# Kernel optimization log

Measured on AMD Instinct MI355X. Metric: run time of the kernel, lower is better.

## Reference

```python
import jax, jax.numpy as jnp
import numpy as np

N_NODES = 100000
N_EDGES = 1600000
F_IN = 128
N_HEADS = 4
F_OUT = 32
NEG_SLOPE = 0.2


def setup_inputs() -> dict:
    key = jax.random.key(0)
    k_feat, k_src, k_dst, k_w, k_as, k_ad, k_res = jax.random.split(key, 7)
    feat = jax.random.normal(k_feat, (N_NODES, F_IN), dtype=jnp.float32)
    src = jax.random.randint(k_src, (N_EDGES,), 0, N_NODES, dtype=jnp.int32)
    dst = jax.random.randint(k_dst, (N_EDGES,), 0, N_NODES, dtype=jnp.int32)
    s = 1.0 / np.sqrt(F_IN)
    W = jax.random.normal(k_w, (F_IN, N_HEADS * F_OUT), dtype=jnp.float32) * s
    att_src = jax.random.normal(k_as, (N_HEADS, F_OUT), dtype=jnp.float32) * 0.1
    att_dst = jax.random.normal(k_ad, (N_HEADS, F_OUT), dtype=jnp.float32) * 0.1
    W_res = jax.random.normal(k_res, (F_IN, N_HEADS * F_OUT), dtype=jnp.float32) * s
    return {"feat": feat, "W": W, "att_src": att_src, "att_dst": att_dst,
            "W_res": W_res, "src": src, "dst": dst}


def reference(feat, W, att_src, att_dst, W_res, src, dst):
    N = feat.shape[0]
    H, Fo = att_src.shape
    # shared linear projection (GATConv, bias=False): [N, H, Fo]
    x = (feat @ W).reshape(N, H, Fo)
    # per-node attention logits: [N, H]
    a_s = jnp.einsum('nhf,hf->nh', x, att_src)
    a_d = jnp.einsum('nhf,hf->nh', x, att_dst)
    # edge-wise scores + LeakyReLU: [E, H]
    e = jax.nn.leaky_relu(a_s[src] + a_d[dst], negative_slope=NEG_SLOPE)
    # segment softmax over incoming edges of each dst node
    e_max = jax.ops.segment_max(e, dst, num_segments=N)  # [N, H]
    e_exp = jnp.exp(e - e_max[dst])                       # [E, H]
    denom = jax.ops.segment_sum(e_exp, dst, num_segments=N)  # [N, H]
    alpha = e_exp / denom[dst]                            # [E, H]
    # weighted scatter-add aggregation: [N, H, Fo]
    msg = x[src] * alpha[:, :, None]
    out = jax.ops.segment_sum(msg, dst, num_segments=N)
    # residual projection
    res = (feat @ W_res).reshape(N, H, Fo)
    return out + res
```

## Files before the change

### kernel.cpp

```cpp
#include <hip/hip_runtime.h>
#include <math.h>

#define NN 100000
#define NE 1600000
#define F_IN 128
#define C 128
#define NEG_SLOPE 0.2f
#define SCAN_NB ((NN + 1023) / 1024)
#define PROJ_NB ((NN + 63) / 64)
#define HIST_NB ((NE + 255) / 256)

typedef __attribute__((ext_vector_type(8))) short short8;
typedef __attribute__((ext_vector_type(4))) float f32x4;
typedef __attribute__((ext_vector_type(4))) float floatx4;
typedef __attribute__((ext_vector_type(4))) unsigned short ushortx4;

static __device__ __forceinline__ unsigned short f2bf(float f) {
    unsigned int u = __float_as_uint(f);
    unsigned int r = (u + 0x7fff + ((u >> 16) & 1)) >> 16;
    return (unsigned short)r;
}
static __device__ __forceinline__ float bf2f(unsigned short h) {
    return __uint_as_float((unsigned int)h << 16);
}

__global__ __launch_bounds__(256)
void wconv_kernel(const float* __restrict__ W,
                  const float* __restrict__ Wr,
                  unsigned short* __restrict__ Btf)
{
    int g = blockIdx.x * 256 + threadIdx.x;
    int nt = g >> 8;
    int kc = (g >> 6) & 3;
    int l  = g & 63;
    int n  = nt * 16 + (l & 15);
    int kb = kc * 32 + (l >> 4) * 8;
    unsigned short v[8];
    #pragma unroll
    for (int j = 0; j < 8; ++j) {
        int k = kb + j;
        float f = (n < 128) ? W[(size_t)k * 128 + n] : Wr[(size_t)k * 128 + (n - 128)];
        v[j] = f2bf(f);
    }
    *(short8*)&Btf[(size_t)g * 8] = *(short8*)v;
}

__global__ __launch_bounds__(256)
void proj_hist_kernel(const float* __restrict__ feat,
                      const unsigned short* __restrict__ Btf,
                      const float* __restrict__ att_src,
                      const float* __restrict__ att_dst,
                      const int* __restrict__ dst,
                      unsigned short* __restrict__ xb,
                      unsigned short* __restrict__ resb,
                      float* __restrict__ a_s,
                      float* __restrict__ a_d,
                      int* __restrict__ deg,
                      int* __restrict__ rank)
{
    __shared__ __align__(16) char smem[17408];
    __shared__ __align__(16) unsigned short Bs[16384];
    __shared__ float s_as[64][4];
    __shared__ float s_ad[64][4];
    const int tid = threadIdx.x;

    if (blockIdx.x >= PROJ_NB) {
        int e = (blockIdx.x - PROJ_NB) * 256 + tid;
        if (e < NE) rank[e] = atomicAdd(&deg[dst[e]], 1);
        return;
    }

    unsigned short* As = (unsigned short*)smem;
    const int base = blockIdx.x * 64;

    #pragma unroll
    for (int it = 0; it < 8; ++it) {
        int idx = it * 256 + tid;
        int row = idx >> 5;
        int c4  = idx & 31;
        int n = base + row;
        if (n < NN) {
            floatx4 f = __builtin_nontemporal_load(
                (const floatx4*)&feat[(size_t)n * F_IN + c4 * 4]);
            ushortx4 h;
            h.x = f2bf(f.x); h.y = f2bf(f.y); h.z = f2bf(f.z); h.w = f2bf(f.w);
            *(ushortx4*)&As[row * 136 + c4 * 4] = h;
        }
    }
    #pragma unroll
    for (int it = 0; it < 8; ++it) {
        int idx = it * 256 + tid;
        *(short8*)&Bs[idx * 8] = *(const short8*)&Btf[idx * 8];
    }
    __syncthreads();

    const int l = tid & 63;
    const int w = tid >> 6;
    const int quad = l >> 4;
    const int lo16 = l & 15;

    short8 af[4];
    const int arow = w * 16 + lo16;
    #pragma unroll
    for (int kc = 0; kc < 4; ++kc)
        af[kc] = *(const short8*)&As[arow * 136 + kc * 32 + quad * 8];

    f32x4 acc[16];
    #pragma unroll
    for (int nt = 0; nt < 16; ++nt) acc[nt] = (f32x4){0.f, 0.f, 0.f, 0.f};

    #pragma unroll
    for (int nt = 0; nt < 8; ++nt) {
        const unsigned short* bp = &Bs[(nt * 4) * 512 + l * 8];
        short8 b0 = *(const short8*)&bp[0];
        short8 b1 = *(const short8*)&bp[512];
        short8 b2 = *(const short8*)&bp[1024];
        short8 b3 = *(const short8*)&bp[1536];
        acc[nt] = __builtin_amdgcn_mfma_f32_16x16x32_bf16(af[0], b0, acc[nt], 0, 0, 0);
        acc[nt] = __builtin_amdgcn_mfma_f32_16x16x32_bf16(af[1], b1, acc[nt], 0, 0, 0);
        acc[nt] = __builtin_amdgcn_mfma_f32_16x16x32_bf16(af[2], b2, acc[nt], 0, 0, 0);
        acc[nt] = __builtin_amdgcn_mfma_f32_16x16x32_bf16(af[3], b3, acc[nt], 0, 0, 0);
    }

    __syncthreads();
    #pragma unroll
    for (int it = 0; it < 8; ++it) {
        int idx = it * 256 + tid;
        *(short8*)&Bs[idx * 8] = *(const short8*)&Btf[16384 + idx * 8];
    }
    __syncthreads();

    #pragma unroll
    for (int nt = 8; nt < 16; ++nt) {
        const unsigned short* bp = &Bs[((nt - 8) * 4) * 512 + l * 8];
        short8 b0 = *(const short8*)&bp[0];
        short8 b1 = *(const short8*)&bp[512];
        short8 b2 = *(const short8*)&bp[1024];
        short8 b3 = *(const short8*)&bp[1536];
        acc[nt] = __builtin_amdgcn_mfma_f32_16x16x32_bf16(af[0], b0, acc[nt], 0, 0, 0);
        acc[nt] = __builtin_amdgcn_mfma_f32_16x16x32_bf16(af[1], b1, acc[nt], 0, 0, 0);
        acc[nt] = __builtin_amdgcn_mfma_f32_16x16x32_bf16(af[2], b2, acc[nt], 0, 0, 0);
        acc[nt] = __builtin_amdgcn_mfma_f32_16x16x32_bf16(af[3], b3, acc[nt], 0, 0, 0);
    }

    float* T2 = (float*)smem + w * (16 * 68);
    const int g  = l >> 4;
    const int cf = (l & 15) * 4;

    #pragma unroll
    for (int p = 0; p < 2; ++p) {
        #pragma unroll
        for (int ntl = 0; ntl < 4; ++ntl) {
            int nt = p * 4 + ntl;
            #pragma unroll
            for (int r = 0; r < 4; ++r)
                T2[(quad * 4 + r) * 68 + ntl * 16 + lo16] = acc[nt][r];
        }
        floatx4 ws4 = *(const floatx4*)&att_src[p * 64 + cf];
        floatx4 wd4 = *(const floatx4*)&att_dst[p * 64 + cf];
        float ps[4], pd[4];
        #pragma unroll
        for (int it = 0; it < 4; ++it) {
            int row = it * 4 + g;
            floatx4 v = *(floatx4*)&T2[row * 68 + cf];
            int node = base + w * 16 + row;
            ushortx4 hh;
            hh.x = f2bf(v.x); hh.y = f2bf(v.y); hh.z = f2bf(v.z); hh.w = f2bf(v.w);
            if (node < NN)
                __builtin_nontemporal_store(hh,
                    (ushortx4*)&xb[(size_t)node * C + p * 64 + cf]);
            ps[it] = v.x * ws4.x + v.y * ws4.y + v.z * ws4.z + v.w * ws4.w;
            pd[it] = v.x * wd4.x + v.y * wd4.y + v.z * wd4.z + v.w * wd4.w;
        }
        #pragma unroll
        for (int it = 0; it < 4; ++it) {
            #pragma unroll
            for (int d = 1; d < 8; d <<= 1) {
                ps[it] += __shfl_xor(ps[it], d, 64);
                pd[it] += __shfl_xor(pd[it], d, 64);
            }
        }
        if ((l & 7) == 0) {
            int hh = p * 2 + ((l & 15) >> 3);
            #pragma unroll
            for (int it = 0; it < 4; ++it) {
                int lr = w * 16 + it * 4 + g;
                s_as[lr][hh] = ps[it];
                s_ad[lr][hh] = pd[it];
            }
        }
    }

    #pragma unroll
    for (int p = 0; p < 2; ++p) {
        #pragma unroll
        for (int ntl = 0; ntl < 4; ++ntl) {
            int nt = 8 + p * 4 + ntl;
            #pragma unroll
            for (int r = 0; r < 4; ++r)
                T2[(quad * 4 + r) * 68 + ntl * 16 + lo16] = acc[nt][r];
        }
        #pragma unroll
        for (int it = 0; it < 4; ++it) {
            int row = it * 4 + g;
            floatx4 v = *(floatx4*)&T2[row * 68 + cf];
            int node = base + w * 16 + row;
            ushortx4 hh;
            hh.x = f2bf(v.x); hh.y = f2bf(v.y); hh.z = f2bf(v.z); hh.w = f2bf(v.w);
            if (node < NN)
                __builtin_nontemporal_store(hh,
                    (ushortx4*)&resb[(size_t)node * C + p * 64 + cf]);
        }
    }

    __syncthreads();
    int idx = blockIdx.x * 256 + tid;
    if (idx < NN * 4) {
        a_s[idx] = ((float*)s_as)[tid];
        a_d[idx] = ((float*)s_ad)[tid];
    }
}

__global__ __launch_bounds__(1024)
void scan1_kernel(const int* __restrict__ deg, int* __restrict__ row_ptr,
                  int* __restrict__ bsum)
{
    __shared__ int wsum[16];
    const int t = threadIdx.x, lane = t & 63, wid = t >> 6;
    const int i = blockIdx.x * 1024 + t;
    int v0 = (i < NN) ? deg[i] : 0;
    int v = v0;
    #pragma unroll
    for (int off = 1; off < 64; off <<= 1) {
        int u = __shfl_up(v, off, 64);
        if (lane >= off) v += u;
    }
    if (lane == 63) wsum[wid] = v;
    __syncthreads();
    if (t == 0) {
        int run = 0;
        #pragma unroll
        for (int s = 0; s < 16; ++s) { int tmp = wsum[s]; wsum[s] = run; run += tmp; }
        bsum[blockIdx.x] = run;
    }
    __syncthreads();
    if (i < NN) row_ptr[i] = wsum[wid] + (v - v0);
}

__global__ __launch_bounds__(128)
void scan2_kernel(int* __restrict__ bsum)
{
    __shared__ int w0;
    const int t = threadIdx.x, lane = t & 63;
    int v0 = (t < SCAN_NB) ? bsum[t] : 0;
    int v = v0;
    #pragma unroll
    for (int off = 1; off < 64; off <<= 1) {
        int u = __shfl_up(v, off, 64);
        if (lane >= off) v += u;
    }
    if (t == 63) w0 = v;
    __syncthreads();
    int excl = (v - v0) + ((t >= 64) ? w0 : 0);
    if (t < SCAN_NB) bsum[t] = excl;
}

__global__ __launch_bounds__(1024)
void scan3_kernel(int* __restrict__ row_ptr, const int* __restrict__ bsum)
{
    const int i = blockIdx.x * 1024 + threadIdx.x;
    if (i < NN) row_ptr[i] = row_ptr[i] + bsum[i >> 10];
    if (i == 0) row_ptr[NN] = NE;
}

__global__ void scatter_kernel(const int* __restrict__ src,
                               const int* __restrict__ dst,
                               const int* __restrict__ rank,
                               const int* __restrict__ row_ptr,
                               int* __restrict__ csr_src)
{
    int e = blockIdx.x * blockDim.x + threadIdx.x;
    if (e < NE)
        csr_src[row_ptr[dst[e]] + rank[e]] = src[e];
}

__global__ __launch_bounds__(256)
void agg_kernel(const unsigned short* __restrict__ xb,
                const unsigned short* __restrict__ resb,
                const float* __restrict__ a_s,
                const float* __restrict__ a_d,
                const int* __restrict__ row_ptr,
                const int* __restrict__ csr_src,
                float* __restrict__ out)
{
    __shared__ float s_alpha[4][64 * 4];
    __shared__ int   s_srcs[4][64];
    const int tid = threadIdx.x;
    const int w = tid >> 6;
    const int l = tid & 63;
    const int n = blockIdx.x * 4 + w;
    if (n >= NN) return;
    const int r0  = row_ptr[n];
    const int deg = row_ptr[n + 1] - r0;

    const int half = l >> 5;
    const int hl   = l & 31;
    const int h    = hl >> 3;

    if (deg == 0) {
        if (half == 0) {
            ushort4 rv = *(const ushort4*)&resb[(size_t)n * C + hl * 4];
            floatx4 o;
            o.x = bf2f(rv.x); o.y = bf2f(rv.y);
            o.z = bf2f(rv.z); o.w = bf2f(rv.w);
            __builtin_nontemporal_store(o, (floatx4*)&out[(size_t)n * C + hl * 4]);
        }
        return;
    }

    const float4 ad4 = *(const float4*)&a_d[n * 4];

    float ax = 0.f, ay = 0.f, az = 0.f, aw = 0.f;
    float dx = 0.f, dy = 0.f, dz = 0.f, dw = 0.f;

    for (int c0 = 0; c0 < deg; c0 += 64) {
        int e = c0 + l;
        int s = 0;
        float4 ex = {0.f, 0.f, 0.f, 0.f};
        if (e < deg) {
            s = csr_src[r0 + e];
            float4 as4 = *(const float4*)&a_s[s * 4];
            float e0 = as4.x + ad4.x, e1 = as4.y + ad4.y;
            float e2 = as4.z + ad4.z, e3 = as4.w + ad4.w;
            e0 = (e0 > 0.f) ? e0 : NEG_SLOPE * e0;
            e1 = (e1 > 0.f) ? e1 : NEG_SLOPE * e1;
            e2 = (e2 > 0.f) ? e2 : NEG_SLOPE * e2;
            e3 = (e3 > 0.f) ? e3 : NEG_SLOPE * e3;
            ex.x = __expf(e0); ex.y = __expf(e1);
            ex.z = __expf(e2); ex.w = __expf(e3);
            dx += ex.x; dy += ex.y; dz += ex.z; dw += ex.w;
        }
        s_srcs[w][l] = s;
        *(float4*)&s_alpha[w][l * 4] = ex;

        int cn = min(64, deg - c0);
        int iters = (cn + 1) >> 1;
        #pragma unroll 2
        for (int i = 0; i < iters; ++i) {
            int ii = i * 2 + half;
            int   si = s_srcs[w][ii];
            float al = s_alpha[w][ii * 4 + h];
            ushort4 uv = *(const ushort4*)&xb[(size_t)si * C + hl * 4];
            ax = fmaf(al, bf2f(uv.x), ax);
            ay = fmaf(al, bf2f(uv.y), ay);
            az = fmaf(al, bf2f(uv.z), az);
            aw = fmaf(al, bf2f(uv.w), aw);
        }
    }

    #pragma unroll
    for (int d = 32; d > 0; d >>= 1) {
        dx += __shfl_xor(dx, d, 64);
        dy += __shfl_xor(dy, d, 64);
        dz += __shfl_xor(dz, d, 64);
        dw += __shfl_xor(dw, d, 64);
    }
    float den = (h == 0) ? dx : (h == 1) ? dy : (h == 2) ? dz : dw;
    float inv = 1.f / den;

    ax += __shfl_xor(ax, 32, 64);
    ay += __shfl_xor(ay, 32, 64);
    az += __shfl_xor(az, 32, 64);
    aw += __shfl_xor(aw, 32, 64);

    if (half == 0) {
        ushort4 rv = *(const ushort4*)&resb[(size_t)n * C + hl * 4];
        floatx4 o;
        o.x = bf2f(rv.x) + ax * inv;
        o.y = bf2f(rv.y) + ay * inv;
        o.z = bf2f(rv.z) + az * inv;
        o.w = bf2f(rv.w) + aw * inv;
        __builtin_nontemporal_store(o, (floatx4*)&out[(size_t)n * C + hl * 4]);
    }
}

extern "C" void kernel_launch(void* const* d_in, const int* in_sizes, int n_in,
                              void* d_out, int out_size, void* d_ws, size_t ws_size,
                              hipStream_t stream)
{
    const float* feat    = (const float*)d_in[0];
    const float* W       = (const float*)d_in[1];
    const float* att_src = (const float*)d_in[2];
    const float* att_dst = (const float*)d_in[3];
    const float* W_res   = (const float*)d_in[4];
    const int*   src     = (const int*)d_in[5];
    const int*   dst     = (const int*)d_in[6];
    float* out = (float*)d_out;

    char* p = (char*)d_ws;
    unsigned short* xb   = (unsigned short*)p; p += (size_t)NN * C * sizeof(unsigned short);
    unsigned short* resb = (unsigned short*)p; p += (size_t)NN * C * sizeof(unsigned short);
    unsigned short* Btf  = (unsigned short*)p; p += (size_t)256 * 128 * sizeof(unsigned short);
    float* a_s = (float*)p;            p += (size_t)NN * 4 * sizeof(float);
    float* a_d = (float*)p;            p += (size_t)NN * 4 * sizeof(float);
    int* deg     = (int*)p;            p += (size_t)NN * sizeof(int);
    int* row_ptr = (int*)p;            p += (size_t)(NN + 1) * sizeof(int);
    int* bsum    = (int*)p;            p += (size_t)256 * sizeof(int);
    int* rank    = (int*)p;            p += (size_t)NE * sizeof(int);
    int* csr_src = (int*)p;            p += (size_t)NE * sizeof(int);

    hipMemsetAsync(deg, 0, (size_t)NN * sizeof(int), stream);

    wconv_kernel<<<16, 256, 0, stream>>>(W, W_res, Btf);
    proj_hist_kernel<<<PROJ_NB + HIST_NB, 256, 0, stream>>>(
        feat, Btf, att_src, att_dst, dst, xb, resb, a_s, a_d, deg, rank);
    scan1_kernel<<<SCAN_NB, 1024, 0, stream>>>(deg, row_ptr, bsum);
    scan2_kernel<<<1, 128, 0, stream>>>(bsum);
    scan3_kernel<<<SCAN_NB, 1024, 0, stream>>>(row_ptr, bsum);
    scatter_kernel<<<(NE + 255) / 256, 256, 0, stream>>>(src, dst, rank, row_ptr, csr_src);
    agg_kernel<<<(NN + 3) / 4, 256, 0, stream>>>(xb, resb, a_s, a_d, row_ptr, csr_src, out);
}
```

Measured before the change: 313.0 us.

## Load projection operands directly from global and widen aggregation gathers to 16 bytes

The projection kernel no longer stages feat and weight tiles in LDS. Each lane loads its bf16 A fragment straight from global memory and reads B fragments from the pre-swizzled weight buffer, which removes several syncthreads and shrinks LDS so more blocks can be resident (launch bounds request 4). The aggregation kernel now has each lane gather 8 bf16 features (16-byte loads) while four edges are processed in parallel per wavefront, reduced afterwards with two cross-lane shuffles. The trade-off is redundant global or L2 reads of the weights by every wave, and more registers in the aggregation loop.

Result: slower. 324.8 us (+3.8%).

```diff
diff --git a/kernel.cpp b/kernel.cpp
--- a/kernel.cpp
+++ b/kernel.cpp
@@ -45,7 +45,7 @@
     *(short8*)&Btf[(size_t)g * 8] = *(short8*)v;
 }
 
-__global__ __launch_bounds__(256)
+__global__ __launch_bounds__(256, 4)
 void proj_hist_kernel(const float* __restrict__ feat,
                       const unsigned short* __restrict__ Btf,
                       const float* __restrict__ att_src,
@@ -58,8 +58,7 @@
                       int* __restrict__ deg,
                       int* __restrict__ rank)
 {
-    __shared__ __align__(16) char smem[17408];
-    __shared__ __align__(16) unsigned short Bs[16384];
+    __shared__ __align__(16) float T2all[4][16 * 68];
     __shared__ float s_as[64][4];
     __shared__ float s_ad[64][4];
     const int tid = threadIdx.x;
@@ -70,48 +69,33 @@
         return;
     }
 
-    unsigned short* As = (unsigned short*)smem;
     const int base = blockIdx.x * 64;
-
-    #pragma unroll
-    for (int it = 0; it < 8; ++it) {
-        int idx = it * 256 + tid;
-        int row = idx >> 5;
-        int c4  = idx & 31;
-        int n = base + row;
-        if (n < NN) {
-            floatx4 f = __builtin_nontemporal_load(
-                (const floatx4*)&feat[(size_t)n * F_IN + c4 * 4]);
-            ushortx4 h;
-            h.x = f2bf(f.x); h.y = f2bf(f.y); h.z = f2bf(f.z); h.w = f2bf(f.w);
-            *(ushortx4*)&As[row * 136 + c4 * 4] = h;
-        }
-    }
-    #pragma unroll
-    for (int it = 0; it < 8; ++it) {
-        int idx = it * 256 + tid;
-        *(short8*)&Bs[idx * 8] = *(const short8*)&Btf[idx * 8];
-    }
-    __syncthreads();
-
     const int l = tid & 63;
     const int w = tid >> 6;
     const int quad = l >> 4;
     const int lo16 = l & 15;
+    const int arow = w * 16 + lo16;
+    const int nclamp = min(base + arow, NN - 1);
 
     short8 af[4];
-    const int arow = w * 16 + lo16;
-    #pragma unroll
-    for (int kc = 0; kc < 4; ++kc)
-        af[kc] = *(const short8*)&As[arow * 136 + kc * 32 + quad * 8];
+    #pragma unroll
+    for (int kc = 0; kc < 4; ++kc) {
+        const float* fp = &feat[(size_t)nclamp * F_IN + kc * 32 + quad * 8];
+        floatx4 f0 = __builtin_nontemporal_load((const floatx4*)fp);
+        floatx4 f1 = __builtin_nontemporal_load((const floatx4*)(fp + 4));
+        unsigned short v[8];
+        v[0] = f2bf(f0.x); v[1] = f2bf(f0.y); v[2] = f2bf(f0.z); v[3] = f2bf(f0.w);
+        v[4] = f2bf(f1.x); v[5] = f2bf(f1.y); v[6] = f2bf(f1.z); v[7] = f2bf(f1.w);
+        af[kc] = *(short8*)v;
+    }
 
     f32x4 acc[16];
     #pragma unroll
     for (int nt = 0; nt < 16; ++nt) acc[nt] = (f32x4){0.f, 0.f, 0.f, 0.f};
 
     #pragma unroll
-    for (int nt = 0; nt < 8; ++nt) {
-        const unsigned short* bp = &Bs[(nt * 4) * 512 + l * 8];
+    for (int nt = 0; nt < 16; ++nt) {
+        const unsigned short* bp = &Btf[(size_t)(nt * 4) * 512 + l * 8];
         short8 b0 = *(const short8*)&bp[0];
         short8 b1 = *(const short8*)&bp[512];
         short8 b2 = *(const short8*)&bp[1024];
@@ -122,28 +106,7 @@
         acc[nt] = __builtin_amdgcn_mfma_f32_16x16x32_bf16(af[3], b3, acc[nt], 0, 0, 0);
     }
 
-    __syncthreads();
-    #pragma unroll
-    for (int it = 0; it < 8; ++it) {
-        int idx = it * 256 + tid;
-        *(short8*)&Bs[idx * 8] = *(const short8*)&Btf[16384 + idx * 8];
-    }
-    __syncthreads();
-
-    #pragma unroll
-    for (int nt = 8; nt < 16; ++nt) {
-        const unsigned short* bp = &Bs[((nt - 8) * 4) * 512 + l * 8];
-        short8 b0 = *(const short8*)&bp[0];
-        short8 b1 = *(const short8*)&bp[512];
-        short8 b2 = *(const short8*)&bp[1024];
-        short8 b3 = *(const short8*)&bp[1536];
-        acc[nt] = __builtin_amdgcn_mfma_f32_16x16x32_bf16(af[0], b0, acc[nt], 0, 0, 0);
-        acc[nt] = __builtin_amdgcn_mfma_f32_16x16x32_bf16(af[1], b1, acc[nt], 0, 0, 0);
-        acc[nt] = __builtin_amdgcn_mfma_f32_16x16x32_bf16(af[2], b2, acc[nt], 0, 0, 0);
-        acc[nt] = __builtin_amdgcn_mfma_f32_16x16x32_bf16(af[3], b3, acc[nt], 0, 0, 0);
-    }
-
-    float* T2 = (float*)smem + w * (16 * 68);
+    float* T2 = T2all[w];
     const int g  = l >> 4;
     const int cf = (l & 15) * 4;
 
@@ -303,24 +266,29 @@
     const int r0  = row_ptr[n];
     const int deg = row_ptr[n + 1] - r0;
 
-    const int half = l >> 5;
-    const int hl   = l & 31;
-    const int h    = hl >> 3;
+    const int quad = l >> 4;
+    const int hl2  = l & 15;
+    const int h    = hl2 >> 2;
 
     if (deg == 0) {
-        if (half == 0) {
-            ushort4 rv = *(const ushort4*)&resb[(size_t)n * C + hl * 4];
-            floatx4 o;
-            o.x = bf2f(rv.x); o.y = bf2f(rv.y);
-            o.z = bf2f(rv.z); o.w = bf2f(rv.w);
-            __builtin_nontemporal_store(o, (floatx4*)&out[(size_t)n * C + hl * 4]);
+        if (quad == 0) {
+            short8 rv = *(const short8*)&resb[(size_t)n * C + hl2 * 8];
+            floatx4 o0, o1;
+            o0.x = bf2f((unsigned short)rv[0]); o0.y = bf2f((unsigned short)rv[1]);
+            o0.z = bf2f((unsigned short)rv[2]); o0.w = bf2f((unsigned short)rv[3]);
+            o1.x = bf2f((unsigned short)rv[4]); o1.y = bf2f((unsigned short)rv[5]);
+            o1.z = bf2f((unsigned short)rv[6]); o1.w = bf2f((unsigned short)rv[7]);
+            __builtin_nontemporal_store(o0, (floatx4*)&out[(size_t)n * C + hl2 * 8]);
+            __builtin_nontemporal_store(o1, (floatx4*)&out[(size_t)n * C + hl2 * 8 + 4]);
         }
         return;
     }
 
     const float4 ad4 = *(const float4*)&a_d[n * 4];
 
-    float ax = 0.f, ay = 0.f, az = 0.f, aw = 0.f;
+    float acc8[8];
+    #pragma unroll
+    for (int j = 0; j < 8; ++j) acc8[j] = 0.f;
     float dx = 0.f, dy = 0.f, dz = 0.f, dw = 0.f;
 
     for (int c0 = 0; c0 < deg; c0 += 64) {
@@ -344,17 +312,21 @@
         *(float4*)&s_alpha[w][l * 4] = ex;
 
         int cn = min(64, deg - c0);
-        int iters = (cn + 1) >> 1;
+        int iters = (cn + 3) >> 2;
         #pragma unroll 2
         for (int i = 0; i < iters; ++i) {
-            int ii = i * 2 + half;
+            int ii = i * 4 + quad;
             int   si = s_srcs[w][ii];
             float al = s_alpha[w][ii * 4 + h];
-            ushort4 uv = *(const ushort4*)&xb[(size_t)si * C + hl * 4];
-            ax = fmaf(al, bf2f(uv.x), ax);
-            ay = fmaf(al, bf2f(uv.y), ay);
-            az = fmaf(al, bf2f(uv.z), az);
-            aw = fmaf(al, bf2f(uv.w), aw);
+            short8 uv = *(const short8*)&xb[(size_t)si * C + hl2 * 8];
+            acc8[0] = fmaf(al, bf2f((unsigned short)uv[0]), acc8[0]);
+            acc8[1] = fmaf(al, bf2f((unsigned short)uv[1]), acc8[1]);
+            acc8[2] = fmaf(al, bf2f((unsigned short)uv[2]), acc8[2]);
+            acc8[3] = fmaf(al, bf2f((unsigned short)uv[3]), acc8[3]);
+            acc8[4] = fmaf(al, bf2f((unsigned short)uv[4]), acc8[4]);
+            acc8[5] = fmaf(al, bf2f((unsigned short)uv[5]), acc8[5]);
+            acc8[6] = fmaf(al, bf2f((unsigned short)uv[6]), acc8[6]);
+            acc8[7] = fmaf(al, bf2f((unsigned short)uv[7]), acc8[7]);
         }
     }
 
@@ -368,19 +340,25 @@
     float den = (h == 0) ? dx : (h == 1) ? dy : (h == 2) ? dz : dw;
     float inv = 1.f / den;
 
-    ax += __shfl_xor(ax, 32, 64);
-    ay += __shfl_xor(ay, 32, 64);
-    az += __shfl_xor(az, 32, 64);
-    aw += __shfl_xor(aw, 32, 64);
-
-    if (half == 0) {
-        ushort4 rv = *(const ushort4*)&resb[(size_t)n * C + hl * 4];
-        floatx4 o;
-        o.x = bf2f(rv.x) + ax * inv;
-        o.y = bf2f(rv.y) + ay * inv;
-        o.z = bf2f(rv.z) + az * inv;
-        o.w = bf2f(rv.w) + aw * inv;
-        __builtin_nontemporal_store(o, (floatx4*)&out[(size_t)n * C + hl * 4]);
+    #pragma unroll
+    for (int j = 0; j < 8; ++j) {
+        acc8[j] += __shfl_xor(acc8[j], 16, 64);
+        acc8[j] += __shfl_xor(acc8[j], 32, 64);
+    }
+
+    if (quad == 0) {
+        short8 rv = *(const short8*)&resb[(size_t)n * C + hl2 * 8];
+        floatx4 o0, o1;
+        o0.x = bf2f((unsigned short)rv[0]) + acc8[0] * inv;
+        o0.y = bf2f((unsigned short)rv[1]) + acc8[1] * inv;
+        o0.z = bf2f((unsigned short)rv[2]) + acc8[2] * inv;
+        o0.w = bf2f((unsigned short)rv[3]) + acc8[3] * inv;
+        o1.x = bf2f((unsigned short)rv[4]) + acc8[4] * inv;
+        o1.y = bf2f((unsigned short)rv[5]) + acc8[5] * inv;
+        o1.z = bf2f((unsigned short)rv[6]) + acc8[6] * inv;
+        o1.w = bf2f((unsigned short)rv[7]) + acc8[7] * inv;
+        __builtin_nontemporal_store(o0, (floatx4*)&out[(size_t)n * C + hl2 * 8]);
+        __builtin_nontemporal_store(o1, (floatx4*)&out[(size_t)n * C + hl2 * 8 + 4]);
     }
 }
 
```

## Replace atomic-histogram CSR build with two-level bucket sort; drop LDS staging in projection

Applied to the files above, without the earlier changes.

The CSR construction no longer relies on global atomics per destination node. It now uses a two-pass bucket sort: per-block LDS histograms over 512-node buckets, a single-block scan, a scatter into packed buckets, then a per-bucket LDS counting sort that writes row_ptr and csr_src. This is meant to remove contended global atomics and random scattered writes. The projection kernel is split off and loads feature and weight fragments straight from global memory instead of staging them in shared memory, which cuts LDS use and raises occupancy. The trade-off is more kernel launches, the serial 256-iteration scan in sortscan, and repeated global reads of the weights.

After: 267.7 us. 1.17x faster.

```diff
diff --git a/kernel.cpp b/kernel.cpp
--- a/kernel.cpp
+++ b/kernel.cpp
@@ -6,9 +6,12 @@
 #define F_IN 128
 #define C 128
 #define NEG_SLOPE 0.2f
-#define SCAN_NB ((NN + 1023) / 1024)
 #define PROJ_NB ((NN + 63) / 64)
-#define HIST_NB ((NE + 255) / 256)
+
+#define NBLK1 256
+#define EPB ((NE + NBLK1 - 1) / NBLK1)
+#define BSHIFT 9
+#define NBUCK ((NN + 511) / 512)
 
 typedef __attribute__((ext_vector_type(8))) short short8;
 typedef __attribute__((ext_vector_type(4))) float f32x4;
@@ -45,73 +48,48 @@
     *(short8*)&Btf[(size_t)g * 8] = *(short8*)v;
 }
 
-__global__ __launch_bounds__(256)
-void proj_hist_kernel(const float* __restrict__ feat,
-                      const unsigned short* __restrict__ Btf,
-                      const float* __restrict__ att_src,
-                      const float* __restrict__ att_dst,
-                      const int* __restrict__ dst,
-                      unsigned short* __restrict__ xb,
-                      unsigned short* __restrict__ resb,
-                      float* __restrict__ a_s,
-                      float* __restrict__ a_d,
-                      int* __restrict__ deg,
-                      int* __restrict__ rank)
-{
-    __shared__ __align__(16) char smem[17408];
-    __shared__ __align__(16) unsigned short Bs[16384];
+__global__ __launch_bounds__(256, 4)
+void proj_kernel(const float* __restrict__ feat,
+                 const unsigned short* __restrict__ Btf,
+                 const float* __restrict__ att_src,
+                 const float* __restrict__ att_dst,
+                 unsigned short* __restrict__ xb,
+                 unsigned short* __restrict__ resb,
+                 float* __restrict__ a_s,
+                 float* __restrict__ a_d)
+{
+    __shared__ __align__(16) float T2all[4][16 * 68];
     __shared__ float s_as[64][4];
     __shared__ float s_ad[64][4];
     const int tid = threadIdx.x;
 
-    if (blockIdx.x >= PROJ_NB) {
-        int e = (blockIdx.x - PROJ_NB) * 256 + tid;
-        if (e < NE) rank[e] = atomicAdd(&deg[dst[e]], 1);
-        return;
-    }
-
-    unsigned short* As = (unsigned short*)smem;
     const int base = blockIdx.x * 64;
-
-    #pragma unroll
-    for (int it = 0; it < 8; ++it) {
-        int idx = it * 256 + tid;
-        int row = idx >> 5;
-        int c4  = idx & 31;
-        int n = base + row;
-        if (n < NN) {
-            floatx4 f = __builtin_nontemporal_load(
-                (const floatx4*)&feat[(size_t)n * F_IN + c4 * 4]);
-            ushortx4 h;
-            h.x = f2bf(f.x); h.y = f2bf(f.y); h.z = f2bf(f.z); h.w = f2bf(f.w);
-            *(ushortx4*)&As[row * 136 + c4 * 4] = h;
-        }
-    }
-    #pragma unroll
-    for (int it = 0; it < 8; ++it) {
-        int idx = it * 256 + tid;
-        *(short8*)&Bs[idx * 8] = *(const short8*)&Btf[idx * 8];
-    }
-    __syncthreads();
-
     const int l = tid & 63;
     const int w = tid >> 6;
     const int quad = l >> 4;
     const int lo16 = l & 15;
+    const int arow = w * 16 + lo16;
+    const int nclamp = min(base + arow, NN - 1);
 
     short8 af[4];
-    const int arow = w * 16 + lo16;
-    #pragma unroll
-    for (int kc = 0; kc < 4; ++kc)
-        af[kc] = *(const short8*)&As[arow * 136 + kc * 32 + quad * 8];
+    #pragma unroll
+    for (int kc = 0; kc < 4; ++kc) {
+        const float* fp = &feat[(size_t)nclamp * F_IN + kc * 32 + quad * 8];
+        floatx4 f0 = __builtin_nontemporal_load((const floatx4*)fp);
+        floatx4 f1 = __builtin_nontemporal_load((const floatx4*)(fp + 4));
+        unsigned short v[8];
+        v[0] = f2bf(f0.x); v[1] = f2bf(f0.y); v[2] = f2bf(f0.z); v[3] = f2bf(f0.w);
+        v[4] = f2bf(f1.x); v[5] = f2bf(f1.y); v[6] = f2bf(f1.z); v[7] = f2bf(f1.w);
+        af[kc] = *(short8*)v;
+    }
 
     f32x4 acc[16];
     #pragma unroll
     for (int nt = 0; nt < 16; ++nt) acc[nt] = (f32x4){0.f, 0.f, 0.f, 0.f};
 
     #pragma unroll
-    for (int nt = 0; nt < 8; ++nt) {
-        const unsigned short* bp = &Bs[(nt * 4) * 512 + l * 8];
+    for (int nt = 0; nt < 16; ++nt) {
+        const unsigned short* bp = &Btf[(size_t)(nt * 4) * 512 + l * 8];
         short8 b0 = *(const short8*)&bp[0];
         short8 b1 = *(const short8*)&bp[512];
         short8 b2 = *(const short8*)&bp[1024];
@@ -122,28 +100,7 @@
         acc[nt] = __builtin_amdgcn_mfma_f32_16x16x32_bf16(af[3], b3, acc[nt], 0, 0, 0);
     }
 
-    __syncthreads();
-    #pragma unroll
-    for (int it = 0; it < 8; ++it) {
-        int idx = it * 256 + tid;
-        *(short8*)&Bs[idx * 8] = *(const short8*)&Btf[16384 + idx * 8];
-    }
-    __syncthreads();
-
-    #pragma unroll
-    for (int nt = 8; nt < 16; ++nt) {
-        const unsigned short* bp = &Bs[((nt - 8) * 4) * 512 + l * 8];
-        short8 b0 = *(const short8*)&bp[0];
-        short8 b1 = *(const short8*)&bp[512];
-        short8 b2 = *(const short8*)&bp[1024];
-        short8 b3 = *(const short8*)&bp[1536];
-        acc[nt] = __builtin_amdgcn_mfma_f32_16x16x32_bf16(af[0], b0, acc[nt], 0, 0, 0);
-        acc[nt] = __builtin_amdgcn_mfma_f32_16x16x32_bf16(af[1], b1, acc[nt], 0, 0, 0);
-        acc[nt] = __builtin_amdgcn_mfma_f32_16x16x32_bf16(af[2], b2, acc[nt], 0, 0, 0);
-        acc[nt] = __builtin_amdgcn_mfma_f32_16x16x32_bf16(af[3], b3, acc[nt], 0, 0, 0);
-    }
-
-    float* T2 = (float*)smem + w * (16 * 68);
+    float* T2 = T2all[w];
     const int g  = l >> 4;
     const int cf = (l & 15) * 4;
 
@@ -221,15 +178,33 @@
     }
 }
 
-__global__ __launch_bounds__(1024)
-void scan1_kernel(const int* __restrict__ deg, int* __restrict__ row_ptr,
-                  int* __restrict__ bsum)
-{
-    __shared__ int wsum[16];
+__global__ __launch_bounds__(256)
+void sort1_kernel(const int* __restrict__ dst, int* __restrict__ counts)
+{
+    __shared__ int h[256];
+    const int tid = threadIdx.x;
+    h[tid] = 0;
+    __syncthreads();
+    const int e0 = blockIdx.x * EPB;
+    const int e1 = min(NE, e0 + EPB);
+    for (int e = e0 + tid; e < e1; e += 256)
+        atomicAdd(&h[dst[e] >> BSHIFT], 1);
+    __syncthreads();
+    counts[blockIdx.x * 256 + tid] = h[tid];
+}
+
+__global__ __launch_bounds__(256)
+void sortscan_kernel(int* __restrict__ counts, int* __restrict__ bucket_base)
+{
+    __shared__ int wsum[4];
     const int t = threadIdx.x, lane = t & 63, wid = t >> 6;
-    const int i = blockIdx.x * 1024 + t;
-    int v0 = (i < NN) ? deg[i] : 0;
-    int v = v0;
+    int run = 0;
+    for (int b = 0; b < NBLK1; ++b) {
+        int v = counts[b * 256 + t];
+        counts[b * 256 + t] = run;
+        run += v;
+    }
+    int v0 = run, v = run;
     #pragma unroll
     for (int off = 1; off < 64; off <<= 1) {
         int u = __shfl_up(v, off, 64);
@@ -238,50 +213,79 @@
     if (lane == 63) wsum[wid] = v;
     __syncthreads();
     if (t == 0) {
-        int run = 0;
-        #pragma unroll
-        for (int s = 0; s < 16; ++s) { int tmp = wsum[s]; wsum[s] = run; run += tmp; }
-        bsum[blockIdx.x] = run;
-    }
-    __syncthreads();
-    if (i < NN) row_ptr[i] = wsum[wid] + (v - v0);
-}
-
-__global__ __launch_bounds__(128)
-void scan2_kernel(int* __restrict__ bsum)
-{
-    __shared__ int w0;
-    const int t = threadIdx.x, lane = t & 63;
-    int v0 = (t < SCAN_NB) ? bsum[t] : 0;
-    int v = v0;
+        int r = 0;
+        #pragma unroll
+        for (int s = 0; s < 4; ++s) { int tmp = wsum[s]; wsum[s] = r; r += tmp; }
+    }
+    __syncthreads();
+    int excl = wsum[wid] + (v - v0);
+    bucket_base[t] = excl;
+    if (t == 255) bucket_base[256] = excl + v0;
+}
+
+__global__ __launch_bounds__(256)
+void sort2_kernel(const int* __restrict__ src, const int* __restrict__ dst,
+                  const int* __restrict__ counts,
+                  const int* __restrict__ bucket_base,
+                  int* __restrict__ bpack)
+{
+    __shared__ int cur[256];
+    const int tid = threadIdx.x;
+    cur[tid] = bucket_base[tid] + counts[blockIdx.x * 256 + tid];
+    __syncthreads();
+    const int e0 = blockIdx.x * EPB;
+    const int e1 = min(NE, e0 + EPB);
+    for (int e = e0 + tid; e < e1; e += 256) {
+        int d = dst[e];
+        int s = src[e];
+        int pos = atomicAdd(&cur[d >> BSHIFT], 1);
+        bpack[pos] = ((d & 511) << 20) | s;
+    }
+}
+
+__global__ __launch_bounds__(512)
+void sort3_kernel(const int* __restrict__ bpack,
+                  const int* __restrict__ bucket_base,
+                  int* __restrict__ row_ptr,
+                  int* __restrict__ csr_src)
+{
+    __shared__ int cnt[512];
+    __shared__ int cur[512];
+    __shared__ int wsum[8];
+    const int t = threadIdx.x, lane = t & 63, wid = t >> 6;
+    const int b = blockIdx.x;
+    const int ebeg = bucket_base[b];
+    const int eend = bucket_base[b + 1];
+    cnt[t] = 0;
+    __syncthreads();
+    for (int e = ebeg + t; e < eend; e += 512)
+        atomicAdd(&cnt[bpack[e] >> 20], 1);
+    __syncthreads();
+    int v0 = cnt[t], v = v0;
     #pragma unroll
     for (int off = 1; off < 64; off <<= 1) {
         int u = __shfl_up(v, off, 64);
         if (lane >= off) v += u;
     }
-    if (t == 63) w0 = v;
-    __syncthreads();
-    int excl = (v - v0) + ((t >= 64) ? w0 : 0);
-    if (t < SCAN_NB) bsum[t] = excl;
-}
-
-__global__ __launch_bounds__(1024)
-void scan3_kernel(int* __restrict__ row_ptr, const int* __restrict__ bsum)
-{
-    const int i = blockIdx.x * 1024 + threadIdx.x;
-    if (i < NN) row_ptr[i] = row_ptr[i] + bsum[i >> 10];
-    if (i == 0) row_ptr[NN] = NE;
-}
-
-__global__ void scatter_kernel(const int* __restrict__ src,
-                               const int* __restrict__ dst,
-                               const int* __restrict__ rank,
-                               const int* __restrict__ row_ptr,
-                               int* __restrict__ csr_src)
-{
-    int e = blockIdx.x * blockDim.x + threadIdx.x;
-    if (e < NE)
-        csr_src[row_ptr[dst[e]] + rank[e]] = src[e];
+    if (lane == 63) wsum[wid] = v;
+    __syncthreads();
+    if (t == 0) {
+        int r = 0;
+        #pragma unroll
+        for (int s = 0; s < 8; ++s) { int tmp = wsum[s]; wsum[s] = r; r += tmp; }
+    }
+    __syncthreads();
+    int excl = wsum[wid] + (v - v0);
+    cur[t] = excl;
+    int n = (b << BSHIFT) + t;
+    if (n < NN) row_ptr[n] = ebeg + excl;
+    if (b == NBUCK - 1 && t == 0) row_ptr[NN] = NE;
+    __syncthreads();
+    for (int e = ebeg + t; e < eend; e += 512) {
+        int p = bpack[e];
+        int pos = atomicAdd(&cur[p >> 20], 1);
+        csr_src[ebeg + pos] = p & 0xFFFFF;
+    }
 }
 
 __global__ __launch_bounds__(256)
@@ -403,20 +407,18 @@
     unsigned short* Btf  = (unsigned short*)p; p += (size_t)256 * 128 * sizeof(unsigned short);
     float* a_s = (float*)p;            p += (size_t)NN * 4 * sizeof(float);
     float* a_d = (float*)p;            p += (size_t)NN * 4 * sizeof(float);
-    int* deg     = (int*)p;            p += (size_t)NN * sizeof(int);
     int* row_ptr = (int*)p;            p += (size_t)(NN + 1) * sizeof(int);
-    int* bsum    = (int*)p;            p += (size_t)256 * sizeof(int);
-    int* rank    = (int*)p;            p += (size_t)NE * sizeof(int);
+    int* counts  = (int*)p;            p += (size_t)NBLK1 * 256 * sizeof(int);
+    int* bucket_base = (int*)p;        p += (size_t)257 * sizeof(int);
+    int* bpack   = (int*)p;            p += (size_t)NE * sizeof(int);
     int* csr_src = (int*)p;            p += (size_t)NE * sizeof(int);
 
-    hipMemsetAsync(deg, 0, (size_t)NN * sizeof(int), stream);
-
     wconv_kernel<<<16, 256, 0, stream>>>(W, W_res, Btf);
-    proj_hist_kernel<<<PROJ_NB + HIST_NB, 256, 0, stream>>>(
-        feat, Btf, att_src, att_dst, dst, xb, resb, a_s, a_d, deg, rank);
-    scan1_kernel<<<SCAN_NB, 1024, 0, stream>>>(deg, row_ptr, bsum);
-    scan2_kernel<<<1, 128, 0, stream>>>(bsum);
-    scan3_kernel<<<SCAN_NB, 1024, 0, stream>>>(row_ptr, bsum);
-    scatter_kernel<<<(NE + 255) / 256, 256, 0, stream>>>(src, dst, rank, row_ptr, csr_src);
+    proj_kernel<<<PROJ_NB, 256, 0, stream>>>(
+        feat, Btf, att_src, att_dst, xb, resb, a_s, a_d);
+    sort1_kernel<<<NBLK1, 256, 0, stream>>>(dst, counts);
+    sortscan_kernel<<<1, 256, 0, stream>>>(counts, bucket_base);
+    sort2_kernel<<<NBLK1, 256, 0, stream>>>(src, dst, counts, bucket_base, bpack);
+    sort3_kernel<<<NBUCK, 512, 0, stream>>>(bpack, bucket_base, row_ptr, csr_src);
     agg_kernel<<<(NN + 3) / 4, 256, 0, stream>>>(xb, resb, a_s, a_d, row_ptr, csr_src, out);
 }
```
